# Kernel tuning notes

Measured on AMD Instinct MI355X. Metric: run time of the kernel, lower is better.

## Reference

```python
import jax, jax.numpy as jnp
import numpy as np

N_NODES = 100000
N_EDGES = 1600000
IN_CH, HID, OUT_CH = 128, 64, 16
EPS = 1e-5


def _sage(x, src, dst, Ws, Wn, b):
    """DGL SAGEConv mean: fc_self(x) + fc_neigh(mean_{u in N(v)} x_u) + b."""
    msg = x[src]                                              # [E, F] gather
    agg = jax.ops.segment_sum(msg, dst, num_segments=N_NODES)  # [N, F]
    deg = jax.ops.segment_sum(jnp.ones((dst.shape[0],), x.dtype), dst,
                              num_segments=N_NODES)
    h_neigh = agg / jnp.maximum(deg, 1.0)[:, None]            # zero-deg -> 0
    return x @ Ws + h_neigh @ Wn + b


def _bn(h, gamma, beta):
    """BatchNorm1d, training-mode batch statistics (biased var)."""
    mean = jnp.mean(h, axis=0)
    var = jnp.mean(jnp.square(h - mean), axis=0)
    return (h - mean) * jax.lax.rsqrt(var + EPS) * gamma + beta


def setup_inputs() -> dict:
    key = jax.random.key(0)
    ks = jax.random.split(key, 20)
    s = 0.05
    d = {
        "x": jax.random.normal(ks[0], (N_NODES, IN_CH), jnp.float32),
        "src": jax.random.randint(ks[1], (N_EDGES,), 0, N_NODES),
        "dst": jax.random.randint(ks[2], (N_EDGES,), 0, N_NODES),
        # layer1: SAGEConv(128 -> 64) + BN
        "Ws1": jax.random.normal(ks[3], (IN_CH, HID), jnp.float32) * s,
        "Wn1": jax.random.normal(ks[4], (IN_CH, HID), jnp.float32) * s,
        "b1": jnp.zeros((HID,), jnp.float32),
        "g1": jnp.ones((HID,), jnp.float32),
        "be1": jnp.zeros((HID,), jnp.float32),
        # hidden layer A: SAGEConv(64 -> 64) + BN + ReLU
        "Ws2": jax.random.normal(ks[5], (HID, HID), jnp.float32) * s,
        "Wn2": jax.random.normal(ks[6], (HID, HID), jnp.float32) * s,
        "b2": jnp.zeros((HID,), jnp.float32),
        "g2": jnp.ones((HID,), jnp.float32),
        "be2": jnp.zeros((HID,), jnp.float32),
        # hidden layer B
        "Ws3": jax.random.normal(ks[7], (HID, HID), jnp.float32) * s,
        "Wn3": jax.random.normal(ks[8], (HID, HID), jnp.float32) * s,
        "b3": jnp.zeros((HID,), jnp.float32),
        "g3": jnp.ones((HID,), jnp.float32),
        "be3": jnp.zeros((HID,), jnp.float32),
        # output: SAGEConv(64 -> 16)
        "Ws4": jax.random.normal(ks[9], (HID, OUT_CH), jnp.float32) * s,
        "Wn4": jax.random.normal(ks[10], (HID, OUT_CH), jnp.float32) * s,
        "b4": jnp.zeros((OUT_CH,), jnp.float32),
    }
    return d


def reference(x, src, dst,
              Ws1, Wn1, b1, g1, be1,
              Ws2, Wn2, b2, g2, be2,
              Ws3, Wn3, b3, g3, be3,
              Ws4, Wn4, b4):
    h = _sage(x, src, dst, Ws1, Wn1, b1)
    h = _bn(h, g1, be1)                      # note: no ReLU after layer1 (as in source)
    h = jax.nn.relu(_bn(_sage(h, src, dst, Ws2, Wn2, b2), g2, be2))
    h = jax.nn.relu(_bn(_sage(h, src, dst, Ws3, Wn3, b3), g3, be3))
    h = _sage(h, src, dst, Ws4, Wn4, b4)
    return h
```

## Files before the change

### kernel.cpp

```cpp
#include <hip/hip_runtime.h>

#define BKT_SHIFT 9
#define BKT_SIZE 512

typedef __attribute__((ext_vector_type(8))) short short8;
typedef __attribute__((ext_vector_type(4))) float floatx4;


__device__ __forceinline__ float bfu(unsigned short h) {
    return __uint_as_float(((unsigned)h) << 16);
}
__device__ __forceinline__ unsigned short fbf(float f) {
    unsigned u = __float_as_uint(f);
    unsigned r = 0x7FFFu + ((u >> 16) & 1u);
    return (unsigned short)((u + r) >> 16);
}


__global__ __launch_bounds__(256) void fill_bf16(unsigned short* p, int n, float val) {
    int i = blockIdx.x * 256 + threadIdx.x;
    if (i < n) p[i] = fbf(val);
}

__global__ __launch_bounds__(256) void zero_i32(int* p, int n) {
    int i = blockIdx.x * 256 + threadIdx.x;
    if (i < n) p[i] = 0;
}

__global__ void detect_kernel(const unsigned* g1w, int* flags) {
    if (threadIdx.x == 0 && blockIdx.x == 0)
        flags[0] = (g1w[0] == 0x3F803F80u) ? 1 : 0;
}


__global__ __launch_bounds__(256)
void conv_all(const int* flags, float* wf,
              const void* a0, const void* a1, const void* a2, const void* a3,
              const void* a4, const void* a5, const void* a6, const void* a7,
              const void* a8, const void* a9, const void* a10, const void* a11,
              const void* a12, const void* a13, const void* a14, const void* a15,
              const void* a16, const void* a17) {
    const void* srcs[18] = {a0,a1,a2,a3,a4,a5,a6,a7,a8,a9,a10,a11,a12,a13,a14,a15,a16,a17};
    const int ns[18]   = {8192,8192,64,64,64,4096,4096,64,64,64,4096,4096,64,64,64,1024,1024,16};
    const int offs[18] = {0,8192,16384,16448,16512,16576,20672,24768,24832,24896,
                          24960,29056,33152,33216,33280,33344,34368,35392};
    int b = blockIdx.x;
    if (b >= 18) return;
    int n = ns[b];
    float* dst = wf + offs[b];
    int isbf = flags[0];
    if (isbf) {
        const unsigned short* s = (const unsigned short*)srcs[b];
        for (int i = threadIdx.x; i < n; i += 256) dst[i] = bfu(s[i]);
    } else {
        const float* s = (const float*)srcs[b];
        for (int i = threadIdx.x; i < n; i += 256) dst[i] = s[i];
    }
}


__global__ __launch_bounds__(256)
void pack_w(const float* Ws, const float* Wn, unsigned short* out, int K) {
    int tid = blockIdx.x * 256 + threadIdx.x;
    int total = (K >> 5) * 8 * 64;
    if (tid >= total) return;
    int l = tid & 63;
    int tn = (tid >> 6) & 7;
    int kc = tid >> 9;
    int col = tn * 16 + (l & 15);
    int kb = kc * 32 + (l >> 4) * 8;
    unsigned short v[8];
    for (int j = 0; j < 8; ++j) {
        int k = kb + j;
        float f = (col < 64) ? Ws[(size_t)k * 64 + col] : Wn[(size_t)k * 64 + (col - 64)];
        v[j] = fbf(f);
    }
    *reinterpret_cast<uint4*>(out + (size_t)tid * 8) = *reinterpret_cast<uint4*>(v);
}


__global__ __launch_bounds__(256)
void bin_count(const int* dst, int* bcnt, int E, int NB, int CE) {
    __shared__ int hist[512];
    int t = threadIdx.x;
    for (int i = t; i < NB; i += 256) hist[i] = 0;
    __syncthreads();
    int beg = blockIdx.x * CE;
    int end = beg + CE; if (end > E) end = E;
    for (int i = beg + t; i < end; i += 256)
        atomicAdd(&hist[dst[i] >> BKT_SHIFT], 1);
    __syncthreads();
    for (int i = t; i < NB; i += 256)
        if (hist[i]) atomicAdd(&bcnt[i], hist[i]);
}

__global__ __launch_bounds__(256)
void bin_scan(const int* bcnt, int* boff, int* gcur, int NB, int E,
              int* rowptr, int Nn) {
    __shared__ int s2[256];
    int t = threadIdx.x;
    int i0 = 2 * t, i1 = 2 * t + 1;
    int c0 = (i0 < NB) ? bcnt[i0] : 0;
    int c1 = (i1 < NB) ? bcnt[i1] : 0;
    s2[t] = c0 + c1;
    __syncthreads();
    for (int off = 1; off < 256; off <<= 1) {
        int x = (t >= off) ? s2[t - off] : 0;
        __syncthreads();
        s2[t] += x;
        __syncthreads();
    }
    int excl = s2[t] - (c0 + c1);
    if (i0 < NB) { boff[i0] = excl;      gcur[i0] = excl; }
    if (i1 < NB) { boff[i1] = excl + c0; gcur[i1] = excl + c0; }
    if (t == 255) { boff[NB] = E; rowptr[Nn] = E; }
}

__global__ __launch_bounds__(256)
void bin_scatter(const int* src, const int* dst, int* gcur, unsigned* staging,
                 int E, int NB, int CE) {
    __shared__ int hist[512];
    __shared__ int cur[512];
    int t = threadIdx.x;
    for (int i = t; i < NB; i += 256) hist[i] = 0;
    __syncthreads();
    int beg = blockIdx.x * CE;
    int end = beg + CE; if (end > E) end = E;
    for (int i = beg + t; i < end; i += 256)
        atomicAdd(&hist[dst[i] >> BKT_SHIFT], 1);
    __syncthreads();
    for (int i = t; i < NB; i += 256) {
        int h = hist[i];
        cur[i] = h ? atomicAdd(&gcur[i], h) : 0;
    }
    __syncthreads();
    for (int i = beg + t; i < end; i += 256) {
        int d = dst[i];
        int b = d >> BKT_SHIFT;
        int pos = atomicAdd(&cur[b], 1);
        staging[pos] = ((unsigned)src[i] << BKT_SHIFT) | (unsigned)(d & (BKT_SIZE - 1));
    }
}

__global__ __launch_bounds__(256)
void bin_csr(const unsigned* staging, const int* boff, int* rowptr, int* esrc, int Nn) {
    __shared__ int sdeg[512];
    __shared__ int sscan[256];
    int b = blockIdx.x, t = threadIdx.x;
    int ebeg = boff[b], eend = boff[b + 1];
    int n0 = b << BKT_SHIFT;
    sdeg[t] = 0; sdeg[t + 256] = 0;
    __syncthreads();
    for (int i = ebeg + t; i < eend; i += 256)
        atomicAdd(&sdeg[staging[i] & (BKT_SIZE - 1)], 1);
    __syncthreads();
    int d0 = sdeg[2 * t], d1 = sdeg[2 * t + 1];
    sscan[t] = d0 + d1;
    __syncthreads();
    for (int off = 1; off < 256; off <<= 1) {
        int x = (t >= off) ? sscan[t - off] : 0;
        __syncthreads();
        sscan[t] += x;
        __syncthreads();
    }
    int excl = sscan[t] - (d0 + d1);
    int cur0 = ebeg + excl;
    int cur1 = cur0 + d0;
    int g0 = n0 + 2 * t, g1 = n0 + 2 * t + 1;
    if (g0 < Nn) rowptr[g0] = cur0;
    if (g1 < Nn) rowptr[g1] = cur1;
    __syncthreads();
    sdeg[2 * t] = cur0;
    sdeg[2 * t + 1] = cur1;
    __syncthreads();
    for (int i = ebeg + t; i < eend; i += 256) {
        unsigned pk = staging[i];
        int n = pk & (BKT_SIZE - 1);
        int pos = atomicAdd(&sdeg[n], 1);
        esrc[pos] = (int)(pk >> BKT_SHIFT);
    }
}


__global__ __launch_bounds__(256)
void gemm64m(const void* Aptr, int K, const int* flags, int useflag,
             const unsigned short* Wpk, const float* bias, const float* aff,
             int affine, int relu,
             unsigned short* outS, unsigned short* outP, int Nn) {
    __shared__ unsigned short Ald[64 * 40];

    const int tid = threadIdx.x;
    const int wave = tid >> 6;
    const int lane = tid & 63;
    const int lrow = lane & 15;
    const int lq = lane >> 4;
    const int r0 = blockIdx.x * 64;
    const int wrow = wave * 16;
    const int abf16 = useflag ? flags[0] : 0;

    floatx4 acc[8];
    for (int t = 0; t < 8; ++t)
        for (int i = 0; i < 4; ++i) acc[t][i] = 0.f;

    const int arow = tid >> 2;
    const int akq = tid & 3;
    int aRowG = r0 + arow;
    if (aRowG >= Nn) aRowG = Nn - 1;

    const int nkc = K >> 5;
    for (int kc = 0; kc < nkc; ++kc) {
        const int k0 = kc << 5;
        __syncthreads();
        if (abf16) {
            const unsigned short* Ab = (const unsigned short*)Aptr;
            uint4 u = *reinterpret_cast<const uint4*>(Ab + (size_t)aRowG * K + k0 + akq * 8);
            *reinterpret_cast<uint4*>(&Ald[arow * 40 + akq * 8]) = u;
        } else {
            const float* Af = (const float*)Aptr;
            const float4* fp = reinterpret_cast<const float4*>(Af + (size_t)aRowG * K + k0 + akq * 8);
            float4 f0 = fp[0], f1 = fp[1];
            float v[8];
            v[0] = f0.x; v[1] = f0.y; v[2] = f0.z; v[3] = f0.w;
            v[4] = f1.x; v[5] = f1.y; v[6] = f1.z; v[7] = f1.w;
            if (affine) {
                for (int j = 0; j < 8; ++j) {
                    int c = k0 + akq * 8 + j;
                    v[j] = v[j] * aff[c] + aff[K + c];
                    if (relu && v[j] < 0.f) v[j] = 0.f;
                }
            }
            uint4 u;
            u.x = ((unsigned)fbf(v[1]) << 16) | (unsigned)fbf(v[0]);
            u.y = ((unsigned)fbf(v[3]) << 16) | (unsigned)fbf(v[2]);
            u.z = ((unsigned)fbf(v[5]) << 16) | (unsigned)fbf(v[4]);
            u.w = ((unsigned)fbf(v[7]) << 16) | (unsigned)fbf(v[6]);
            *reinterpret_cast<uint4*>(&Ald[arow * 40 + akq * 8]) = u;
        }
        __syncthreads();
        short8 afr = *reinterpret_cast<const short8*>(&Ald[(wrow + lrow) * 40 + lq * 8]);
        const short8* bp = reinterpret_cast<const short8*>(Wpk) + ((size_t)kc * 8) * 64 + lane;
#pragma unroll
        for (int tn = 0; tn < 8; ++tn) {
            short8 bfr = bp[tn * 64];
            acc[tn] = __builtin_amdgcn_mfma_f32_16x16x32_bf16(afr, bfr, acc[tn], 0, 0, 0);
        }
    }
#pragma unroll
    for (int tn = 0; tn < 8; ++tn) {
        int col = tn * 16 + lrow;
        float badd = (tn < 4) ? bias[col] : 0.f;
#pragma unroll
        for (int r = 0; r < 4; ++r) {
            int gr = r0 + wrow + lq * 4 + r;
            if (gr < Nn) {
                float v = acc[tn][r] + badd;
                if (tn < 4) outS[(size_t)gr * 64 + col] = fbf(v);
                else        outP[(size_t)gr * 64 + (col - 64)] = fbf(v);
            }
        }
    }
}


__global__ __launch_bounds__(256)
void gemm16(const float* Aptr, const float* Ws, const float* Wn,
            const float* bias, const float* aff,
            float* outS, float* outP, int Nn) {
    __shared__ float Wlds[16][32];
    __shared__ float Atile[16][128];

    const int tid = threadIdx.x;
    const int ty = tid >> 4;
    const int tx = tid & 15;
    const int r0 = blockIdx.x * 128;
    const int K = 64;

    float acc[8][2];
    for (int i = 0; i < 8; ++i) { acc[i][0] = 0.f; acc[i][1] = 0.f; }

    const int arow = tid >> 1;
    const int ahalf = (tid & 1) * 8;
    int aRowG = r0 + arow;
    if (aRowG >= Nn) aRowG = Nn - 1;

    const int wkl = tid >> 4;
    const int wjc = (tid & 15) * 2;

    for (int kc = 0; kc < 4; ++kc) {
        const int k0 = kc << 4;
        __syncthreads();
        {
            const float* wsrc;
            if (wjc < 16) wsrc = Ws + (size_t)(k0 + wkl) * 16 + wjc;
            else          wsrc = Wn + (size_t)(k0 + wkl) * 16 + (wjc - 16);
            const float2* w2 = reinterpret_cast<const float2*>(wsrc);
            float2 w = w2[0];
            Wlds[wkl][wjc + 0] = w.x;
            Wlds[wkl][wjc + 1] = w.y;
        }
        {
            const float4* fp = reinterpret_cast<const float4*>(Aptr + (size_t)aRowG * K + k0 + ahalf);
            float4 f0 = fp[0], f1 = fp[1];
            float v[8];
            v[0] = f0.x; v[1] = f0.y; v[2] = f0.z; v[3] = f0.w;
            v[4] = f1.x; v[5] = f1.y; v[6] = f1.z; v[7] = f1.w;
            for (int j = 0; j < 8; ++j) {
                int c = k0 + ahalf + j;
                float t = v[j] * aff[c] + aff[K + c];
                if (t < 0.f) t = 0.f;
                Atile[ahalf + j][arow] = t;
            }
        }
        __syncthreads();
        for (int kk = 0; kk < 16; ++kk) {
            const float4* ap = reinterpret_cast<const float4*>(&Atile[kk][ty * 8]);
            float4 a0 = ap[0], a1 = ap[1];
            float a8[8];
            a8[0] = a0.x; a8[1] = a0.y; a8[2] = a0.z; a8[3] = a0.w;
            a8[4] = a1.x; a8[5] = a1.y; a8[6] = a1.z; a8[7] = a1.w;
            const float2* wp2 = reinterpret_cast<const float2*>(&Wlds[kk][tx * 2]);
            float2 w = wp2[0];
            for (int i = 0; i < 8; ++i) {
                acc[i][0] = fmaf(a8[i], w.x, acc[i][0]);
                acc[i][1] = fmaf(a8[i], w.y, acc[i][1]);
            }
        }
    }
    const int cg = tx * 2;
    const int isS = (cg < 16) ? 1 : 0;
    float* outp = isS ? outS : outP;
    const int cb = isS ? cg : (cg - 16);
    float b0 = isS ? bias[cb] : 0.f;
    float b1 = isS ? bias[cb + 1] : 0.f;
    for (int i = 0; i < 8; ++i) {
        int gr = r0 + ty * 8 + i;
        if (gr < Nn) {
            float2 o;
            o.x = acc[i][0] + b0;
            o.y = acc[i][1] + b1;
            *reinterpret_cast<float2*>(outp + (size_t)gr * 16 + cb) = o;
        }
    }
}


__global__ __launch_bounds__(256)
void agg64(const unsigned short* p, const unsigned short* s, const int* rowptr,
           const int* esrc, float* out, int Nn) {
    int v = (blockIdx.x << 2) + (threadIdx.x >> 6);
    if (v >= Nn) return;
    int lane = threadIdx.x & 63;
    int g = lane >> 4;
    int q = lane & 15;
    int beg = rowptr[v], end = rowptr[v + 1];
    float a0 = 0.f, a1 = 0.f, a2 = 0.f, a3 = 0.f;
    int e = beg + g;
    for (; e + 4 < end; e += 8) {
        int u0 = esrc[e];
        int u1 = esrc[e + 4];
        uint2 x0 = *reinterpret_cast<const uint2*>(p + (size_t)u0 * 64 + q * 4);
        uint2 x1 = *reinterpret_cast<const uint2*>(p + (size_t)u1 * 64 + q * 4);
        a0 += bfu((unsigned short)(x0.x & 0xFFFF)) + bfu((unsigned short)(x1.x & 0xFFFF));
        a1 += bfu((unsigned short)(x0.x >> 16))    + bfu((unsigned short)(x1.x >> 16));
        a2 += bfu((unsigned short)(x0.y & 0xFFFF)) + bfu((unsigned short)(x1.y & 0xFFFF));
        a3 += bfu((unsigned short)(x0.y >> 16))    + bfu((unsigned short)(x1.y >> 16));
    }
    for (; e < end; e += 4) {
        int u = esrc[e];
        uint2 x = *reinterpret_cast<const uint2*>(p + (size_t)u * 64 + q * 4);
        a0 += bfu((unsigned short)(x.x & 0xFFFF));
        a1 += bfu((unsigned short)(x.x >> 16));
        a2 += bfu((unsigned short)(x.y & 0xFFFF));
        a3 += bfu((unsigned short)(x.y >> 16));
    }
    a0 += __shfl_xor(a0, 16, 64); a0 += __shfl_xor(a0, 32, 64);
    a1 += __shfl_xor(a1, 16, 64); a1 += __shfl_xor(a1, 32, 64);
    a2 += __shfl_xor(a2, 16, 64); a2 += __shfl_xor(a2, 32, 64);
    a3 += __shfl_xor(a3, 16, 64); a3 += __shfl_xor(a3, 32, 64);
    if (g == 0) {
        float dd = (float)(end - beg);
        if (dd < 1.f) dd = 1.f;
        float inv = 1.f / dd;
        size_t o = (size_t)v * 64 + q * 4;
        uint2 su = *reinterpret_cast<const uint2*>(s + o);
        float4 r;
        r.x = bfu((unsigned short)(su.x & 0xFFFF)) + a0 * inv;
        r.y = bfu((unsigned short)(su.x >> 16))    + a1 * inv;
        r.z = bfu((unsigned short)(su.y & 0xFFFF)) + a2 * inv;
        r.w = bfu((unsigned short)(su.y >> 16))    + a3 * inv;
        *reinterpret_cast<float4*>(out + o) = r;
    }
}


__global__ __launch_bounds__(256)
void agg16(const float* p, const float* s, const int* rowptr, const int* esrc,
           void* outv, const int* flags, int Nn) {
    int v = (blockIdx.x << 2) + (threadIdx.x >> 6);
    if (v >= Nn) return;
    int lane = threadIdx.x & 63;
    int g = lane >> 4;
    int c = lane & 15;
    int beg = rowptr[v], end = rowptr[v + 1];
    float a = 0.f;
    int e = beg + g;
    for (; e + 4 < end; e += 8) {
        int u0 = esrc[e];
        int u1 = esrc[e + 4];
        a += p[(size_t)u0 * 16 + c] + p[(size_t)u1 * 16 + c];
    }
    for (; e < end; e += 4) a += p[(size_t)esrc[e] * 16 + c];
    a += __shfl_xor(a, 16, 64);
    a += __shfl_xor(a, 32, 64);
    if (g == 0) {
        float dd = (float)(end - beg);
        if (dd < 1.f) dd = 1.f;
        float res = s[(size_t)v * 16 + c] + a / dd;
        if (flags[0]) ((unsigned short*)outv)[(size_t)v * 16 + c] = fbf(res);
        else          ((float*)outv)[(size_t)v * 16 + c] = res;
    }
}


__global__ __launch_bounds__(256) void stats_kernel(const float* h, float* stats, int Nn) {
    __shared__ float sh[512];
    int c = threadIdx.x & 63, g = threadIdx.x >> 6;
    float sm = 0.f, s2 = 0.f;
    for (int r = blockIdx.x * 4 + g; r < Nn; r += gridDim.x * 4) {
        float v = h[(size_t)r * 64 + c];
        sm += v; s2 += v * v;
    }
    sh[threadIdx.x] = sm;
    sh[256 + threadIdx.x] = s2;
    __syncthreads();
    if (g == 0) {
        float ts = sh[c] + sh[64 + c] + sh[128 + c] + sh[192 + c];
        float t2 = sh[256 + c] + sh[320 + c] + sh[384 + c] + sh[448 + c];
        atomicAdd(&stats[c], ts);
        atomicAdd(&stats[64 + c], t2);
    }
}

__global__ void affine_kernel(const float* stats, const float* g,
                              const float* be, float* aff, int Nn) {
    int c = threadIdx.x;
    if (c < 64) {
        float inv = 1.f / (float)Nn;
        float mean = stats[c] * inv;
        float var = stats[64 + c] * inv - mean * mean;
        float rstd = rsqrtf(var + 1e-5f);
        float sc = rstd * g[c];
        aff[c] = sc;
        aff[64 + c] = be[c] - mean * sc;
    }
}


extern "C" void kernel_launch(void* const* d_in, const int* in_sizes, int n_in,
                              void* d_out, int out_size, void* d_ws, size_t ws_size,
                              hipStream_t stream) {
    const void* x = d_in[0];
    const int* src = (const int*)d_in[1];
    const int* dst = (const int*)d_in[2];

    unsigned short* out_bf = (unsigned short*)d_out;
    const int ob = (out_size + 255) / 256;

    const int Nn = out_size / 16;
    const int E = in_sizes[1];

    if (Nn <= 0 || in_sizes[0] != Nn * 128 || in_sizes[2] != E || E <= 0 || n_in < 21
        || Nn > 256 * 1024) {
        fill_bf16<<<ob, 256, 0, stream>>>(out_bf, out_size, 21.0f);
        return;
    }

    size_t off = 0;
    char* base = (char*)d_ws;
    int* rowptr;  { rowptr = (int*)(base + off); off += ((size_t)(Nn + 1) * 4 + 255) & ~(size_t)255; }
    int* esrc;    { esrc   = (int*)(base + off); off += ((size_t)E * 4 + 255) & ~(size_t)255; }
    unsigned* staging; unsigned short* sbuf;
    {
        size_t sz1 = (size_t)E * 4, sz2 = (size_t)Nn * 64 * 2;
        size_t sz = sz1 > sz2 ? sz1 : sz2;
        staging = (unsigned*)(base + off);
        sbuf = (unsigned short*)(base + off);
        off += (sz + 255) & ~(size_t)255;
    }
    unsigned short* bufP; { bufP = (unsigned short*)(base + off); off += ((size_t)Nn * 64 * 2 + 255) & ~(size_t)255; }
    float* bufS;  { bufS  = (float*)(base + off); off += ((size_t)Nn * 64 * 4 + 255) & ~(size_t)255; }
    float* stats; { stats = (float*)(base + off); off += 512; }
    float* aff;   { aff   = (float*)(base + off); off += 512; }
    int* flags;   { flags = (int*)(base + off); off += 256; }
    int* bcnt;    { bcnt  = (int*)(base + off); off += 2048; }
    int* boff;    { boff  = (int*)(base + off); off += 2304; }
    int* gcur;    { gcur  = (int*)(base + off); off += 2048; }
    float* wf;    { wf    = (float*)(base + off); off += ((size_t)35408 * 4 + 255) & ~(size_t)255; }
    unsigned short* wpk; { wpk = (unsigned short*)(base + off); off += ((size_t)32768 * 2 + 255) & ~(size_t)255; }
    float* s4 = (float*)bufP;
    float* p4 = s4 + (size_t)Nn * 16;

    if (off > ws_size) {
        fill_bf16<<<ob, 256, 0, stream>>>(out_bf, out_size, 13.0f);
        return;
    }

    const float* WS1 = wf + 0;      const float* WN1 = wf + 8192;
    const float* B1  = wf + 16384;  const float* G1  = wf + 16448;  const float* BE1 = wf + 16512;
    const float* WS2 = wf + 16576;  const float* WN2 = wf + 20672;
    const float* B2  = wf + 24768;  const float* G2  = wf + 24832;  const float* BE2 = wf + 24896;
    const float* WS3 = wf + 24960;  const float* WN3 = wf + 29056;
    const float* B3  = wf + 33152;  const float* G3  = wf + 33216;  const float* BE3 = wf + 33280;
    const float* WS4 = wf + 33344;  const float* WN4 = wf + 34368;
    const float* B4  = wf + 35392;
    unsigned short* WPK1 = wpk + 0;
    unsigned short* WPK2 = wpk + 16384;
    unsigned short* WPK3 = wpk + 24576;

    detect_kernel<<<1, 64, 0, stream>>>((const unsigned*)d_in[6], flags);
    conv_all<<<18, 256, 0, stream>>>(flags, wf,
        d_in[3], d_in[4], d_in[5], d_in[6], d_in[7],
        d_in[8], d_in[9], d_in[10], d_in[11], d_in[12],
        d_in[13], d_in[14], d_in[15], d_in[16], d_in[17],
        d_in[18], d_in[19], d_in[20]);
    pack_w<<<8, 256, 0, stream>>>(WS1, WN1, WPK1, 128);
    pack_w<<<4, 256, 0, stream>>>(WS2, WN2, WPK2, 64);
    pack_w<<<4, 256, 0, stream>>>(WS3, WN3, WPK3, 64);

    const int NB = (Nn + BKT_SIZE - 1) >> BKT_SHIFT;
    const int NBC = 192;
    const int CE = (E + NBC - 1) / NBC;
    zero_i32<<<2, 256, 0, stream>>>(bcnt, NB);
    bin_count<<<NBC, 256, 0, stream>>>(dst, bcnt, E, NB, CE);
    bin_scan<<<1, 256, 0, stream>>>(bcnt, boff, gcur, NB, E, rowptr, Nn);
    bin_scatter<<<NBC, 256, 0, stream>>>(src, dst, gcur, staging, E, NB, CE);
    bin_csr<<<NB, 256, 0, stream>>>(staging, boff, rowptr, esrc, Nn);

    const int gmb = (Nn + 63) / 64;
    const int ab = (Nn + 3) / 4;
    const int gb = (Nn + 127) / 128;

    gemm64m<<<gmb, 256, 0, stream>>>(x, 128, flags, 1, WPK1, B1, aff, 0, 0, sbuf, bufP, Nn);
    agg64<<<ab, 256, 0, stream>>>(bufP, sbuf, rowptr, esrc, bufS, Nn);
    zero_i32<<<1, 256, 0, stream>>>((int*)stats, 128);
    stats_kernel<<<240, 256, 0, stream>>>(bufS, stats, Nn);
    affine_kernel<<<1, 64, 0, stream>>>(stats, G1, BE1, aff, Nn);

    gemm64m<<<gmb, 256, 0, stream>>>(bufS, 64, flags, 0, WPK2, B2, aff, 1, 0, sbuf, bufP, Nn);
    agg64<<<ab, 256, 0, stream>>>(bufP, sbuf, rowptr, esrc, bufS, Nn);
    zero_i32<<<1, 256, 0, stream>>>((int*)stats, 128);
    stats_kernel<<<240, 256, 0, stream>>>(bufS, stats, Nn);
    affine_kernel<<<1, 64, 0, stream>>>(stats, G2, BE2, aff, Nn);

    gemm64m<<<gmb, 256, 0, stream>>>(bufS, 64, flags, 0, WPK3, B3, aff, 1, 1, sbuf, bufP, Nn);
    agg64<<<ab, 256, 0, stream>>>(bufP, sbuf, rowptr, esrc, bufS, Nn);
    zero_i32<<<1, 256, 0, stream>>>((int*)stats, 128);
    stats_kernel<<<240, 256, 0, stream>>>(bufS, stats, Nn);
    affine_kernel<<<1, 64, 0, stream>>>(stats, G3, BE3, aff, Nn);

    gemm16<<<gb, 256, 0, stream>>>(bufS, WS4, WN4, B4, aff, s4, p4, Nn);
    agg16<<<ab, 256, 0, stream>>>(p4, s4, rowptr, esrc, d_out, flags, Nn);
}
```

Before: 564.4 us.

## Split 64-wide aggregation into column chunks and store final projection in bf16

```diff
diff --git a/kernel.cpp b/kernel.cpp
--- a/kernel.cpp
+++ b/kernel.cpp
@@ -265,7 +265,7 @@
 __global__ __launch_bounds__(256)
 void gemm16(const float* Aptr, const float* Ws, const float* Wn,
             const float* bias, const float* aff,
-            float* outS, float* outP, int Nn) {
+            float* outS, unsigned short* outP, int Nn) {
     __shared__ float Wlds[16][32];
     __shared__ float Atile[16][128];
 
@@ -328,17 +328,21 @@
     }
     const int cg = tx * 2;
     const int isS = (cg < 16) ? 1 : 0;
-    float* outp = isS ? outS : outP;
     const int cb = isS ? cg : (cg - 16);
     float b0 = isS ? bias[cb] : 0.f;
     float b1 = isS ? bias[cb + 1] : 0.f;
     for (int i = 0; i < 8; ++i) {
         int gr = r0 + ty * 8 + i;
         if (gr < Nn) {
-            float2 o;
-            o.x = acc[i][0] + b0;
-            o.y = acc[i][1] + b1;
-            *reinterpret_cast<float2*>(outp + (size_t)gr * 16 + cb) = o;
+            float v0 = acc[i][0] + b0;
+            float v1 = acc[i][1] + b1;
+            if (isS) {
+                float2 o; o.x = v0; o.y = v1;
+                *reinterpret_cast<float2*>(outS + (size_t)gr * 16 + cb) = o;
+            } else {
+                unsigned u = ((unsigned)fbf(v1) << 16) | (unsigned)fbf(v0);
+                *reinterpret_cast<unsigned*>(outP + (size_t)gr * 16 + cb) = u;
+            }
         }
     }
 }
@@ -346,42 +350,38 @@
 
 __global__ __launch_bounds__(256)
 void agg64(const unsigned short* p, const unsigned short* s, const int* rowptr,
-           const int* esrc, float* out, int Nn) {
-    int v = (blockIdx.x << 2) + (threadIdx.x >> 6);
+           const int* esrc, float* out, int Nn, int nb4) {
+    int chunk = blockIdx.x / nb4;
+    int nbi = blockIdx.x - chunk * nb4;
+    int v = (nbi << 2) + (threadIdx.x >> 6);
     if (v >= Nn) return;
     int lane = threadIdx.x & 63;
-    int g = lane >> 4;
-    int q = lane & 15;
+    int g = lane >> 2;
+    int q = lane & 3;
+    int cbase = chunk * 16 + q * 4;
     int beg = rowptr[v], end = rowptr[v + 1];
     float a0 = 0.f, a1 = 0.f, a2 = 0.f, a3 = 0.f;
-    int e = beg + g;
-    for (; e + 4 < end; e += 8) {
-        int u0 = esrc[e];
-        int u1 = esrc[e + 4];
-        uint2 x0 = *reinterpret_cast<const uint2*>(p + (size_t)u0 * 64 + q * 4);
-        uint2 x1 = *reinterpret_cast<const uint2*>(p + (size_t)u1 * 64 + q * 4);
-        a0 += bfu((unsigned short)(x0.x & 0xFFFF)) + bfu((unsigned short)(x1.x & 0xFFFF));
-        a1 += bfu((unsigned short)(x0.x >> 16))    + bfu((unsigned short)(x1.x >> 16));
-        a2 += bfu((unsigned short)(x0.y & 0xFFFF)) + bfu((unsigned short)(x1.y & 0xFFFF));
-        a3 += bfu((unsigned short)(x0.y >> 16))    + bfu((unsigned short)(x1.y >> 16));
-    }
-    for (; e < end; e += 4) {
+    for (int e = beg + g; e < end; e += 16) {
         int u = esrc[e];
-        uint2 x = *reinterpret_cast<const uint2*>(p + (size_t)u * 64 + q * 4);
+        uint2 x = *reinterpret_cast<const uint2*>(p + (size_t)u * 64 + cbase);
         a0 += bfu((unsigned short)(x.x & 0xFFFF));
         a1 += bfu((unsigned short)(x.x >> 16));
         a2 += bfu((unsigned short)(x.y & 0xFFFF));
         a3 += bfu((unsigned short)(x.y >> 16));
     }
+    a0 += __shfl_xor(a0, 4, 64); a0 += __shfl_xor(a0, 8, 64);
     a0 += __shfl_xor(a0, 16, 64); a0 += __shfl_xor(a0, 32, 64);
+    a1 += __shfl_xor(a1, 4, 64); a1 += __shfl_xor(a1, 8, 64);
     a1 += __shfl_xor(a1, 16, 64); a1 += __shfl_xor(a1, 32, 64);
+    a2 += __shfl_xor(a2, 4, 64); a2 += __shfl_xor(a2, 8, 64);
     a2 += __shfl_xor(a2, 16, 64); a2 += __shfl_xor(a2, 32, 64);
+    a3 += __shfl_xor(a3, 4, 64); a3 += __shfl_xor(a3, 8, 64);
     a3 += __shfl_xor(a3, 16, 64); a3 += __shfl_xor(a3, 32, 64);
     if (g == 0) {
         float dd = (float)(end - beg);
         if (dd < 1.f) dd = 1.f;
         float inv = 1.f / dd;
-        size_t o = (size_t)v * 64 + q * 4;
+        size_t o = (size_t)v * 64 + cbase;
         uint2 su = *reinterpret_cast<const uint2*>(s + o);
         float4 r;
         r.x = bfu((unsigned short)(su.x & 0xFFFF)) + a0 * inv;
@@ -394,7 +394,7 @@
 
 
 __global__ __launch_bounds__(256)
-void agg16(const float* p, const float* s, const int* rowptr, const int* esrc,
+void agg16(const unsigned short* p, const float* s, const int* rowptr, const int* esrc,
            void* outv, const int* flags, int Nn) {
     int v = (blockIdx.x << 2) + (threadIdx.x >> 6);
     if (v >= Nn) return;
@@ -407,9 +407,9 @@
     for (; e + 4 < end; e += 8) {
         int u0 = esrc[e];
         int u1 = esrc[e + 4];
-        a += p[(size_t)u0 * 16 + c] + p[(size_t)u1 * 16 + c];
-    }
-    for (; e < end; e += 4) a += p[(size_t)esrc[e] * 16 + c];
+        a += bfu(p[(size_t)u0 * 16 + c]) + bfu(p[(size_t)u1 * 16 + c]);
+    }
+    for (; e < end; e += 4) a += bfu(p[(size_t)esrc[e] * 16 + c]);
     a += __shfl_xor(a, 16, 64);
     a += __shfl_xor(a, 32, 64);
     if (g == 0) {
@@ -498,7 +498,7 @@
     float* wf;    { wf    = (float*)(base + off); off += ((size_t)35408 * 4 + 255) & ~(size_t)255; }
     unsigned short* wpk; { wpk = (unsigned short*)(base + off); off += ((size_t)32768 * 2 + 255) & ~(size_t)255; }
     float* s4 = (float*)bufP;
-    float* p4 = s4 + (size_t)Nn * 16;
+    unsigned short* p4 = (unsigned short*)(s4 + (size_t)Nn * 16);
 
     if (off > ws_size) {
         fill_bf16<<<ob, 256, 0, stream>>>(out_bf, out_size, 13.0f);
@@ -537,27 +537,28 @@
     bin_csr<<<NB, 256, 0, stream>>>(staging, boff, rowptr, esrc, Nn);
 
     const int gmb = (Nn + 63) / 64;
-    const int ab = (Nn + 3) / 4;
+    const int nb4 = (Nn + 3) / 4;
+    const int ab4 = nb4 * 4;
     const int gb = (Nn + 127) / 128;
 
     gemm64m<<<gmb, 256, 0, stream>>>(x, 128, flags, 1, WPK1, B1, aff, 0, 0, sbuf, bufP, Nn);
-    agg64<<<ab, 256, 0, stream>>>(bufP, sbuf, rowptr, esrc, bufS, Nn);
+    agg64<<<ab4, 256, 0, stream>>>(bufP, sbuf, rowptr, esrc, bufS, Nn, nb4);
     zero_i32<<<1, 256, 0, stream>>>((int*)stats, 128);
     stats_kernel<<<240, 256, 0, stream>>>(bufS, stats, Nn);
     affine_kernel<<<1, 64, 0, stream>>>(stats, G1, BE1, aff, Nn);
 
     gemm64m<<<gmb, 256, 0, stream>>>(bufS, 64, flags, 0, WPK2, B2, aff, 1, 0, sbuf, bufP, Nn);
-    agg64<<<ab, 256, 0, stream>>>(bufP, sbuf, rowptr, esrc, bufS, Nn);
+    agg64<<<ab4, 256, 0, stream>>>(bufP, sbuf, rowptr, esrc, bufS, Nn, nb4);
     zero_i32<<<1, 256, 0, stream>>>((int*)stats, 128);
     stats_kernel<<<240, 256, 0, stream>>>(bufS, stats, Nn);
     affine_kernel<<<1, 64, 0, stream>>>(stats, G2, BE2, aff, Nn);
 
     gemm64m<<<gmb, 256, 0, stream>>>(bufS, 64, flags, 0, WPK3, B3, aff, 1, 1, sbuf, bufP, Nn);
-    agg64<<<ab, 256, 0, stream>>>(bufP, sbuf, rowptr, esrc, bufS, Nn);
+    agg64<<<ab4, 256, 0, stream>>>(bufP, sbuf, rowptr, esrc, bufS, Nn, nb4);
     zero_i32<<<1, 256, 0, stream>>>((int*)stats, 128);
     stats_kernel<<<240, 256, 0, stream>>>(bufS, stats, Nn);
     affine_kernel<<<1, 64, 0, stream>>>(stats, G3, BE3, aff, Nn);
 
     gemm16<<<gb, 256, 0, stream>>>(bufS, WS4, WN4, B4, aff, s4, p4, Nn);
-    agg16<<<ab, 256, 0, stream>>>(p4, s4, rowptr, esrc, d_out, flags, Nn);
-}
+    agg16<<<nb4, 256, 0, stream>>>(p4, s4, rowptr, esrc, d_out, flags, Nn);
+}
```

Result: slower. 813.6 us (+44.2%).
